# Performance work log

Hardware: AMD Instinct MI355X
Metric: run time of the kernel (lower is better)

Reference implementation:

```python
import jax, jax.numpy as jnp
import numpy as np

N = 50000
E = 800000
EPS = 1e-5


def graph_conv(x, src, dst, ew, W_rel, b_rel, W_root):
    # PyG GraphConv (aggr='add'): lin_rel(sum_j e_ij * x_j) + lin_root(x_i)
    msg = x[src] * ew[:, None]                      # [E, F_in]
    agg = jax.ops.segment_sum(msg, dst, num_segments=N)  # [N, F_in]
    return agg @ W_rel.T + b_rel + x @ W_root.T


def batchnorm_relu(h, gamma, beta):
    mu = jnp.mean(h, axis=0)
    var = jnp.mean(jnp.square(h - mu), axis=0)
    hn = (h - mu) * jax.lax.rsqrt(var + EPS)
    return jax.nn.relu(hn * gamma + beta)


def setup_inputs() -> dict:
    key = jax.random.key(0)
    ks = jax.random.split(key, 16)
    d_in, h, d_out = 128, 256, 64

    def lin(k, fo, fi):
        return jax.random.normal(k, (fo, fi), jnp.float32) * (1.0 / np.sqrt(fi))

    return {
        "x": jax.random.normal(ks[0], (N, d_in), jnp.float32),
        "edge_index": jax.random.randint(ks[1], (2, E), 0, N, jnp.int32),
        "edge_weight": jax.random.uniform(ks[2], (E,), jnp.float32),
        "Wr0": lin(ks[3], h, d_in), "br0": jnp.zeros((h,), jnp.float32), "Wt0": lin(ks[4], h, d_in),
        "g0": jnp.ones((h,), jnp.float32), "be0": jnp.zeros((h,), jnp.float32),
        "Wr1": lin(ks[5], h, h), "br1": jnp.zeros((h,), jnp.float32), "Wt1": lin(ks[6], h, h),
        "g1": jnp.ones((h,), jnp.float32), "be1": jnp.zeros((h,), jnp.float32),
        "Wr2": lin(ks[7], d_out, h), "br2": jnp.zeros((d_out,), jnp.float32), "Wt2": lin(ks[8], d_out, h),
    }


def reference(x, edge_index, edge_weight, Wr0, br0, Wt0, g0, be0,
              Wr1, br1, Wt1, g1, be1, Wr2, br2, Wt2):
    src, dst = edge_index[0], edge_index[1]
    h = graph_conv(x, src, dst, edge_weight, Wr0, br0, Wt0)
    h = batchnorm_relu(h, g0, be0)
    h = graph_conv(h, src, dst, edge_weight, Wr1, br1, Wt1)
    h = batchnorm_relu(h, g1, be1)
    return graph_conv(h, src, dst, edge_weight, Wr2, br2, Wt2)
```

## Files before the change

### kernel.cpp

```cpp
#include <hip/hip_runtime.h>
#include <cstddef>
#include <cstdint>

#define SCAN_B 512

using bf16x8 = __attribute__((ext_vector_type(8))) short;
using f32x4  = __attribute__((ext_vector_type(4))) float;

__device__ __forceinline__ unsigned short f2bf(float f) {
    unsigned int u = __builtin_bit_cast(unsigned int, f);
    return (unsigned short)((u + 0x7FFFu + ((u >> 16) & 1u)) >> 16);
}
__device__ __forceinline__ float bf2f(unsigned short b) {
    unsigned int u = ((unsigned int)b) << 16;
    return __builtin_bit_cast(float, u);
}
__device__ __forceinline__ float i2f(int i) { return __builtin_bit_cast(float, i); }
__device__ __forceinline__ float u2f(unsigned int u) { return __builtin_bit_cast(float, u); }
__device__ __forceinline__ void gload_lds16(const void* g, void* l) {
    __builtin_amdgcn_global_load_lds((const __attribute__((address_space(1))) void*)g,
                                     (__attribute__((address_space(3))) void*)l, 16, 0, 0);
}

__global__ void hist_conv_k(const int* __restrict__ dst, int* __restrict__ counts,
                            int* __restrict__ rank, int E, int histBlocks,
                            const float* __restrict__ x, const float* __restrict__ Wr0,
                            const float* __restrict__ Wt0, const float* __restrict__ Wr1,
                            const float* __restrict__ Wt1, const float* __restrict__ Wr2,
                            const float* __restrict__ Wt2, unsigned short* __restrict__ x_bf,
                            unsigned short* __restrict__ Wr0b, unsigned short* __restrict__ Wt0b,
                            unsigned short* __restrict__ Wr1b, unsigned short* __restrict__ Wt1b,
                            unsigned short* __restrict__ Wr2b, unsigned short* __restrict__ Wt2b,
                            int n4x) {
    if ((int)blockIdx.x < histBlocks) {
        int e = blockIdx.x * 256 + threadIdx.x;
        if (e < E) rank[e] = atomicAdd(&counts[dst[e]], 1);
        return;
    }
    int j = (blockIdx.x - histBlocks) * 256 + threadIdx.x;
    const float* s;
    unsigned short* d;
    if (j < n4x) { s = x; d = x_bf; }
    else {
        j -= n4x;
        if (j < 8192) { s = Wr0; d = Wr0b; }
        else { j -= 8192;
        if (j < 8192) { s = Wt0; d = Wt0b; }
        else { j -= 8192;
        if (j < 16384) { s = Wr1; d = Wr1b; }
        else { j -= 16384;
        if (j < 16384) { s = Wt1; d = Wt1b; }
        else { j -= 16384;
        if (j < 4096) { s = Wr2; d = Wr2b; }
        else { j -= 4096;
        if (j >= 4096) return;
        s = Wt2; d = Wt2b; } } } } }
    }
    float4 v = reinterpret_cast<const float4*>(s)[j];
    ushort4 o;
    o.x = f2bf(v.x); o.y = f2bf(v.y); o.z = f2bf(v.z); o.w = f2bf(v.w);
    reinterpret_cast<ushort4*>(d)[j] = o;
}

__global__ void scan1_k(const int* __restrict__ counts, int* __restrict__ partial,
                        int* __restrict__ blocksum, int Nn) {
    __shared__ int sh[SCAN_B];
    int i = blockIdx.x * SCAN_B + threadIdx.x;
    int v = (i < Nn) ? counts[i] : 0;
    sh[threadIdx.x] = v;
    __syncthreads();
    for (int off = 1; off < SCAN_B; off <<= 1) {
        int t = (threadIdx.x >= (unsigned)off) ? sh[threadIdx.x - off] : 0;
        __syncthreads();
        sh[threadIdx.x] += t;
        __syncthreads();
    }
    if (i < Nn) partial[i] = sh[threadIdx.x];
    if (threadIdx.x == SCAN_B - 1) blocksum[blockIdx.x] = sh[threadIdx.x];
}

__global__ void scan2_k(int* __restrict__ blocksum, int nb) {
    __shared__ int sh[256];
    int v = (threadIdx.x < (unsigned)nb) ? blocksum[threadIdx.x] : 0;
    sh[threadIdx.x] = v;
    __syncthreads();
    for (int off = 1; off < 256; off <<= 1) {
        int t = (threadIdx.x >= (unsigned)off) ? sh[threadIdx.x - off] : 0;
        __syncthreads();
        sh[threadIdx.x] += t;
        __syncthreads();
    }
    if (threadIdx.x < (unsigned)nb) blocksum[threadIdx.x] = sh[threadIdx.x];
}

__global__ void scan3_k(const int* __restrict__ partial, const int* __restrict__ blocksum,
                        int* __restrict__ offsets, int Nn) {
    int i = blockIdx.x * SCAN_B + threadIdx.x;
    if (i >= Nn) return;
    int add = (blockIdx.x > 0) ? blocksum[blockIdx.x - 1] : 0;
    offsets[i + 1] = partial[i] + add;
    if (i == 0) offsets[0] = 0;
}

__global__ void fill2_k(const int* __restrict__ src, const int* __restrict__ dst,
                        const float* __restrict__ ew, const int* __restrict__ offsets,
                        const int* __restrict__ rank, int2* __restrict__ e_sw, int E) {
    int e = blockIdx.x * blockDim.x + threadIdx.x;
    if (e >= E) return;
    int d = dst[e];
    int pos = offsets[d] + rank[e];
    e_sw[pos] = make_int2(src[e], __builtin_bit_cast(int, ew[e]));
}

template<int F>
__global__ void gather_bf_k(const unsigned short* __restrict__ x, const int* __restrict__ offsets,
                            const int2* __restrict__ e_sw, unsigned short* __restrict__ agg, int Nn) {
    int wid = __builtin_amdgcn_readfirstlane((blockIdx.x * blockDim.x + threadIdx.x) >> 6);
    int lane = threadIdx.x & 63;
    if (wid >= Nn) return;
    int p = offsets[wid], end = offsets[wid + 1];
    const char* xb = (const char*)x;
    if constexpr (F == 256) {
        const unsigned loff = lane * 8u;
        float a0 = 0.f, a1 = 0.f, a2 = 0.f, a3 = 0.f;
        for (; p + 8 <= end; p += 8) {
            int2 ee[8];
            #pragma unroll
            for (int i = 0; i < 8; ++i) ee[i] = e_sw[p + i];
            uint2 vv[8];
            #pragma unroll
            for (int i = 0; i < 8; ++i)
                vv[i] = *reinterpret_cast<const uint2*>(xb + ((unsigned)ee[i].x * 512u + loff));
            #pragma unroll
            for (int i = 0; i < 8; ++i) {
                float w = i2f(ee[i].y);
                a0 += w * u2f(vv[i].x << 16); a1 += w * u2f(vv[i].x & 0xFFFF0000u);
                a2 += w * u2f(vv[i].y << 16); a3 += w * u2f(vv[i].y & 0xFFFF0000u);
            }
        }
        for (; p < end; ++p) {
            int2 e0 = e_sw[p];
            uint2 v0 = *reinterpret_cast<const uint2*>(xb + ((unsigned)e0.x * 512u + loff));
            float w = i2f(e0.y);
            a0 += w * u2f(v0.x << 16); a1 += w * u2f(v0.x & 0xFFFF0000u);
            a2 += w * u2f(v0.y << 16); a3 += w * u2f(v0.y & 0xFFFF0000u);
        }
        uint2 o;
        o.x = (unsigned)f2bf(a0) | ((unsigned)f2bf(a1) << 16);
        o.y = (unsigned)f2bf(a2) | ((unsigned)f2bf(a3) << 16);
        *reinterpret_cast<uint2*>(agg + (size_t)wid * 256 + lane * 4) = o;
    } else {
        const unsigned loff = lane * 4u;
        float a0 = 0.f, a1 = 0.f;
        for (; p + 8 <= end; p += 8) {
            int2 ee[8];
            #pragma unroll
            for (int i = 0; i < 8; ++i) ee[i] = e_sw[p + i];
            unsigned vv[8];
            #pragma unroll
            for (int i = 0; i < 8; ++i)
                vv[i] = *reinterpret_cast<const unsigned*>(xb + ((unsigned)ee[i].x * 256u + loff));
            #pragma unroll
            for (int i = 0; i < 8; ++i) {
                float w = i2f(ee[i].y);
                a0 += w * u2f(vv[i] << 16); a1 += w * u2f(vv[i] & 0xFFFF0000u);
            }
        }
        for (; p < end; ++p) {
            int2 e0 = e_sw[p];
            unsigned v0 = *reinterpret_cast<const unsigned*>(xb + ((unsigned)e0.x * 256u + loff));
            float w = i2f(e0.y);
            a0 += w * u2f(v0 << 16); a1 += w * u2f(v0 & 0xFFFF0000u);
        }
        unsigned o = (unsigned)f2bf(a0) | ((unsigned)f2bf(a1) << 16);
        *reinterpret_cast<unsigned*>(agg + (size_t)wid * 128 + lane * 2) = o;
    }
}

__global__ void gather_out_k(const unsigned short* __restrict__ t, const float* __restrict__ root,
                             const int* __restrict__ offsets, const int2* __restrict__ e_sw,
                             float* __restrict__ out, int Nn) {
    int gt = blockIdx.x * blockDim.x + threadIdx.x;
    int node = gt >> 4;
    int li = gt & 15;
    if (node >= Nn) return;
    int p = offsets[node], end = offsets[node + 1];
    const char* tb = (const char*)t;
    const unsigned loff = li * 8u;
    float a0 = 0.f, a1 = 0.f, a2 = 0.f, a3 = 0.f;
    for (; p + 8 <= end; p += 8) {
        int2 ee[8];
        #pragma unroll
        for (int i = 0; i < 8; ++i) ee[i] = e_sw[p + i];
        uint2 vv[8];
        #pragma unroll
        for (int i = 0; i < 8; ++i)
            vv[i] = *reinterpret_cast<const uint2*>(tb + ((unsigned)ee[i].x * 128u + loff));
        #pragma unroll
        for (int i = 0; i < 8; ++i) {
            float w = i2f(ee[i].y);
            a0 += w * u2f(vv[i].x << 16); a1 += w * u2f(vv[i].x & 0xFFFF0000u);
            a2 += w * u2f(vv[i].y << 16); a3 += w * u2f(vv[i].y & 0xFFFF0000u);
        }
    }
    for (; p < end; ++p) {
        int2 e0 = e_sw[p];
        uint2 v0 = *reinterpret_cast<const uint2*>(tb + ((unsigned)e0.x * 128u + loff));
        float w = i2f(e0.y);
        a0 += w * u2f(v0.x << 16); a1 += w * u2f(v0.x & 0xFFFF0000u);
        a2 += w * u2f(v0.y << 16); a3 += w * u2f(v0.y & 0xFFFF0000u);
    }
    float4 r = *reinterpret_cast<const float4*>(root + (size_t)node * 64 + li * 4);
    float4 o = make_float4(r.x + a0, r.y + a1, r.z + a2, r.w + a3);
    *reinterpret_cast<float4*>(out + (size_t)node * 64 + li * 4) = o;
}

template<int K, int O, int BM, int BN, int MODE>
__global__ __launch_bounds__(512, 4) void gemm_mfma_k(
        const unsigned short* __restrict__ A, const unsigned short* __restrict__ Wa,
        const unsigned short* __restrict__ X, const unsigned short* __restrict__ Wb,
        const float* __restrict__ bias, unsigned short* __restrict__ out_bf,
        float* __restrict__ out_f, float* __restrict__ sums, float* __restrict__ sumsq,
        int Nn) {
    constexpr int MI = BM / 32;
    constexpr int OJ = BN / 64;
    constexpr int KSTEPS = K / 64;
    constexpr int NT = (MODE == 0 ? 2 : 1) * KSTEPS;
    constexpr int ACH = BM / 64;
    constexpr int BCH = BN / 64;
    __shared__ unsigned short As[2][BM * 64];
    __shared__ unsigned short Bs[2][BN * 64];
    const int tid = threadIdx.x;
    const int w = tid >> 6, l = tid & 63;
    const int wr = w >> 2, wc = w & 3;
    const int lrow = l & 15, kgrp = l >> 4;
    int bx = blockIdx.x;
    bx = (bx & 7) * (gridDim.x >> 3) + (bx >> 3);
    const int m0 = bx * BM;
    const int n0 = blockIdx.y * BN;

    auto stage = [&](int buf, int t) {
        int ph = t / KSTEPS;
        int k0 = (t % KSTEPS) * 64;
        const unsigned short* Ap = (MODE == 0 && ph) ? X : A;
        const unsigned short* Wp = (MODE == 0 && ph) ? Wb : Wa;
        #pragma unroll
        for (int i = 0; i < ACH; ++i) {
            int c = i * 512 + tid;
            int row = c >> 3, slot = c & 7;
            gload_lds16(Ap + (size_t)(m0 + row) * K + k0 + ((slot ^ (row & 7)) << 3),
                        &As[buf][(i * 512 + w * 64) * 8]);
        }
        #pragma unroll
        for (int i = 0; i < BCH; ++i) {
            int c = i * 512 + tid;
            int row = c >> 3, slot = c & 7;
            gload_lds16(Wp + (size_t)(n0 + row) * K + k0 + ((slot ^ (row & 7)) << 3),
                        &Bs[buf][(i * 512 + w * 64) * 8]);
        }
    };

    f32x4 acc[MI][OJ];
    #pragma unroll
    for (int i = 0; i < MI; ++i)
        #pragma unroll
        for (int j = 0; j < OJ; ++j) {
            f32x4 z = {0.f, 0.f, 0.f, 0.f};
            acc[i][j] = z;
        }

    stage(0, 0);
    __syncthreads();
    #pragma unroll
    for (int t = 0; t < NT; ++t) {
        const int cur = t & 1;
        if (t + 1 < NT) stage(cur ^ 1, t + 1);
        #pragma unroll
        for (int ks = 0; ks < 2; ++ks) {
            bf16x8 a[MI], b[OJ];
            #pragma unroll
            for (int mi = 0; mi < MI; ++mi) {
                int row = wr * 64 + mi * 16 + lrow;
                int slot = (ks * 4 + kgrp) ^ (row & 7);
                a[mi] = *reinterpret_cast<const bf16x8*>(&As[cur][row * 64 + slot * 8]);
            }
            #pragma unroll
            for (int oj = 0; oj < OJ; ++oj) {
                int row = wc * 32 + oj * 16 + lrow;
                int slot = (ks * 4 + kgrp) ^ (row & 7);
                b[oj] = *reinterpret_cast<const bf16x8*>(&Bs[cur][row * 64 + slot * 8]);
            }
            #pragma unroll
            for (int mi = 0; mi < MI; ++mi)
                #pragma unroll
                for (int oj = 0; oj < OJ; ++oj)
                    acc[mi][oj] = __builtin_amdgcn_mfma_f32_16x16x32_bf16(
                        a[mi], b[oj], acc[mi][oj], 0, 0, 0);
        }
        __syncthreads();
    }

    if constexpr (MODE == 0) {
        #pragma unroll
        for (int oj = 0; oj < OJ; ++oj) {
            int col = n0 + wc * 32 + oj * 16 + lrow;
            float bcol = bias[col];
            float s = 0.f, q = 0.f;
            #pragma unroll
            for (int mi = 0; mi < MI; ++mi) {
                #pragma unroll
                for (int r = 0; r < 4; ++r) {
                    int row = m0 + wr * 64 + mi * 16 + kgrp * 4 + r;
                    float v = acc[mi][oj][r] + bcol;
                    if (row < Nn) {
                        out_bf[(size_t)row * O + col] = f2bf(v);
                        s += v; q += v * v;
                    }
                }
            }
            s += __shfl_xor(s, 16, 64); q += __shfl_xor(q, 16, 64);
            s += __shfl_xor(s, 32, 64); q += __shfl_xor(q, 32, 64);
            if (kgrp == 0) {
                atomicAdd(&sums[col], s);
                atomicAdd(&sumsq[col], q);
            }
        }
    } else {
        #pragma unroll
        for (int oj = 0; oj < OJ; ++oj) {
            int col = n0 + wc * 32 + oj * 16 + lrow;
            #pragma unroll
            for (int mi = 0; mi < MI; ++mi) {
                #pragma unroll
                for (int r = 0; r < 4; ++r) {
                    int row = m0 + wr * 64 + mi * 16 + kgrp * 4 + r;
                    if (row < Nn) {
                        if (col < 64)
                            out_bf[(size_t)row * 64 + col] = f2bf(acc[mi][oj][r]);
                        else
                            out_f[(size_t)row * 64 + (col - 64)] = acc[mi][oj][r] + bias[col - 64];
                    }
                }
            }
        }
    }
}

__global__ void bn_relu_bf_k(const unsigned short* __restrict__ h, const float* __restrict__ sums,
                             const float* __restrict__ sumsq, const float* __restrict__ g,
                             const float* __restrict__ be, unsigned short* __restrict__ hb,
                             float invN, int total4) {
    int t = blockIdx.x * blockDim.x + threadIdx.x;
    if (t >= total4) return;
    int f0 = (t & 63) * 4;
    float4 sm = *reinterpret_cast<const float4*>(sums + f0);
    float4 sq = *reinterpret_cast<const float4*>(sumsq + f0);
    float4 gg = *reinterpret_cast<const float4*>(g + f0);
    float4 bb = *reinterpret_cast<const float4*>(be + f0);
    float smv[4] = {sm.x, sm.y, sm.z, sm.w};
    float sqv[4] = {sq.x, sq.y, sq.z, sq.w};
    float ggv[4] = {gg.x, gg.y, gg.z, gg.w};
    float bbv[4] = {bb.x, bb.y, bb.z, bb.w};
    ushort4 v = reinterpret_cast<const ushort4*>(h)[t];
    unsigned short vv[4] = {v.x, v.y, v.z, v.w};
    ushort4 o;
    unsigned short* op = &o.x;
    #pragma unroll
    for (int c = 0; c < 4; ++c) {
        float mu = smv[c] * invN;
        float var = sqv[c] * invN - mu * mu;
        float sc = ggv[c] * rsqrtf(var + 1e-5f);
        float sh = bbv[c] - mu * sc;
        op[c] = f2bf(fmaxf(bf2f(vv[c]) * sc + sh, 0.f));
    }
    reinterpret_cast<ushort4*>(hb)[t] = o;
}

extern "C" void kernel_launch(void* const* d_in, const int* in_sizes, int n_in,
                              void* d_out, int out_size, void* d_ws, size_t ws_size,
                              hipStream_t stream) {
    const float* x   = (const float*)d_in[0];
    const int*   ei  = (const int*)d_in[1];
    const float* ew  = (const float*)d_in[2];
    const float* Wr0 = (const float*)d_in[3];
    const float* br0 = (const float*)d_in[4];
    const float* Wt0 = (const float*)d_in[5];
    const float* g0  = (const float*)d_in[6];
    const float* be0 = (const float*)d_in[7];
    const float* Wr1 = (const float*)d_in[8];
    const float* br1 = (const float*)d_in[9];
    const float* Wt1 = (const float*)d_in[10];
    const float* g1  = (const float*)d_in[11];
    const float* be1 = (const float*)d_in[12];
    const float* Wr2 = (const float*)d_in[13];
    const float* br2 = (const float*)d_in[14];
    const float* Wt2 = (const float*)d_in[15];

    const int E  = in_sizes[2];
    const int Nn = in_sizes[0] / 128;
    const size_t NP = 50176;
    const int* src = ei;
    const int* dst = ei + E;

    unsigned short* x_bf   = (unsigned short*)d_ws;
    unsigned short* agg_bf = x_bf + NP * 128;
    unsigned short* h0N    = agg_bf + NP * 256;
    unsigned short* h1N    = h0N + NP * 256;
    unsigned short* h_bf   = h1N + NP * 256;
    unsigned short* t_bf   = h_bf + NP * 256;
    unsigned short* wbf    = t_bf + NP * 64;
    unsigned short* Wr0b = wbf;
    unsigned short* Wt0b = wbf + 32768;
    unsigned short* Wr1b = wbf + 65536;
    unsigned short* Wt1b = wbf + 131072;
    unsigned short* W2cat = wbf + 196608;
    float* root  = (float*)(wbf + 229376);
    int2*  e_sw  = (int2*)(root + NP * 64);
    float* stats = (float*)(e_sw + E);
    int*   counts  = (int*)(stats + 4096);
    int*   partial = counts + Nn;
    int*   blocksum = partial + Nn;
    int*   rank    = blocksum + 512;
    int*   offsets = rank + E;

    dim3 blk(256);
    const int nbScan = (Nn + SCAN_B - 1) / SCAN_B;
    const float invN = 1.0f / (float)Nn;
    const int n4x = Nn * 32;
    const int histBlocks = (E + 255) / 256;
    const int convBlocks = (n4x + 57344 + 255) / 256;

    hipMemsetAsync(stats, 0, (4096 + (size_t)Nn) * sizeof(float), stream);

    hist_conv_k<<<dim3(histBlocks + convBlocks), blk, 0, stream>>>(
        dst, counts, rank, E, histBlocks,
        x, Wr0, Wt0, Wr1, Wt1, Wr2, Wt2,
        x_bf, Wr0b, Wt0b, Wr1b, Wt1b, W2cat, W2cat + 16384, n4x);
    scan1_k<<<dim3(nbScan), dim3(SCAN_B), 0, stream>>>(counts, partial, blocksum, Nn);
    scan2_k<<<dim3(1), dim3(256), 0, stream>>>(blocksum, nbScan);
    scan3_k<<<dim3(nbScan), dim3(SCAN_B), 0, stream>>>(partial, blocksum, offsets, Nn);
    fill2_k<<<dim3(histBlocks), blk, 0, stream>>>(src, dst, ew, offsets, rank, e_sw, E);

    const int gatherBlocks = (Nn * 64 + 255) / 256;

    gather_bf_k<128><<<dim3(gatherBlocks), blk, 0, stream>>>(x_bf, offsets, e_sw, agg_bf, Nn);
    gemm_mfma_k<128, 256, 128, 128, 0><<<dim3(NP / 128, 2), dim3(512), 0, stream>>>(
        agg_bf, Wr0b, x_bf, Wt0b, br0, h_bf, nullptr, stats + 0, stats + 256, Nn);
    bn_relu_bf_k<<<dim3((Nn * 64 + 255) / 256), blk, 0, stream>>>(
        h_bf, stats + 0, stats + 256, g0, be0, h0N, invN, Nn * 64);

    gather_bf_k<256><<<dim3(gatherBlocks), blk, 0, stream>>>(h0N, offsets, e_sw, agg_bf, Nn);
    gemm_mfma_k<256, 256, 128, 128, 0><<<dim3(NP / 128, 2), dim3(512), 0, stream>>>(
        agg_bf, Wr1b, h0N, Wt1b, br1, h_bf, nullptr, stats + 1024, stats + 1280, Nn);
    bn_relu_bf_k<<<dim3((Nn * 64 + 255) / 256), blk, 0, stream>>>(
        h_bf, stats + 1024, stats + 1280, g1, be1, h1N, invN, Nn * 64);

    gemm_mfma_k<256, 128, 128, 128, 1><<<dim3(NP / 128, 1), dim3(512), 0, stream>>>(
        h1N, W2cat, nullptr, nullptr, br2, t_bf, root, nullptr, nullptr, Nn);
    gather_out_k<<<dim3((Nn * 16 + 255) / 256), blk, 0, stream>>>(
        t_bf, root, offsets, e_sw, (float*)d_out, Nn);
}
```

Before: 304.6 us.

## Fuse BN-ReLU into layer-1 gather, merge scan kernels, shrink GEMM K-tile

The second and third scan kernels become one, with each block summing the preceding block totals itself. The layer-0 BN+ReLU is folded into the layer-1 gather, which normalizes neighbor rows on the fly, while extra blocks in the same launch write the normalized h0N needed by the root GEMM. The GEMM K-step drops from 64 to 32, using half the LDS, one 16-byte load per thread per operand, and a new XOR swizzle. This removes two launches and a dependent read of h0N before the gather, at the cost of recomputing BN per edge element and running more, shorter K iterations with more barriers.

```diff
diff --git a/kernel.cpp b/kernel.cpp
--- a/kernel.cpp
+++ b/kernel.cpp
@@ -79,26 +79,21 @@
     if (threadIdx.x == SCAN_B - 1) blocksum[blockIdx.x] = sh[threadIdx.x];
 }
 
-__global__ void scan2_k(int* __restrict__ blocksum, int nb) {
-    __shared__ int sh[256];
-    int v = (threadIdx.x < (unsigned)nb) ? blocksum[threadIdx.x] : 0;
-    sh[threadIdx.x] = v;
+__global__ void scan3b_k(const int* __restrict__ partial, const int* __restrict__ blocksum,
+                         int* __restrict__ offsets, int Nn) {
+    __shared__ int add_s;
+    int bx = blockIdx.x;
+    if (threadIdx.x < 64) {
+        int s = 0;
+        for (int j = threadIdx.x; j < bx; j += 64) s += blocksum[j];
+        #pragma unroll
+        for (int off = 32; off > 0; off >>= 1) s += __shfl_down(s, off, 64);
+        if (threadIdx.x == 0) add_s = s;
+    }
     __syncthreads();
-    for (int off = 1; off < 256; off <<= 1) {
-        int t = (threadIdx.x >= (unsigned)off) ? sh[threadIdx.x - off] : 0;
-        __syncthreads();
-        sh[threadIdx.x] += t;
-        __syncthreads();
-    }
-    if (threadIdx.x < (unsigned)nb) blocksum[threadIdx.x] = sh[threadIdx.x];
-}
-
-__global__ void scan3_k(const int* __restrict__ partial, const int* __restrict__ blocksum,
-                        int* __restrict__ offsets, int Nn) {
-    int i = blockIdx.x * SCAN_B + threadIdx.x;
+    int i = bx * SCAN_B + threadIdx.x;
     if (i >= Nn) return;
-    int add = (blockIdx.x > 0) ? blocksum[blockIdx.x - 1] : 0;
-    offsets[i + 1] = partial[i] + add;
+    offsets[i + 1] = partial[i] + add_s;
     if (i == 0) offsets[0] = 0;
 }
 
@@ -107,74 +102,128 @@
                         const int* __restrict__ rank, int2* __restrict__ e_sw, int E) {
     int e = blockIdx.x * blockDim.x + threadIdx.x;
     if (e >= E) return;
-    int d = dst[e];
-    int pos = offsets[d] + rank[e];
+    int pos = offsets[dst[e]] + rank[e];
     e_sw[pos] = make_int2(src[e], __builtin_bit_cast(int, ew[e]));
 }
 
-template<int F>
-__global__ void gather_bf_k(const unsigned short* __restrict__ x, const int* __restrict__ offsets,
+__global__ void gather128_k(const unsigned short* __restrict__ x, const int* __restrict__ offsets,
                             const int2* __restrict__ e_sw, unsigned short* __restrict__ agg, int Nn) {
     int wid = __builtin_amdgcn_readfirstlane((blockIdx.x * blockDim.x + threadIdx.x) >> 6);
     int lane = threadIdx.x & 63;
     if (wid >= Nn) return;
     int p = offsets[wid], end = offsets[wid + 1];
     const char* xb = (const char*)x;
-    if constexpr (F == 256) {
-        const unsigned loff = lane * 8u;
-        float a0 = 0.f, a1 = 0.f, a2 = 0.f, a3 = 0.f;
-        for (; p + 8 <= end; p += 8) {
-            int2 ee[8];
+    const unsigned loff = lane * 4u;
+    float a0 = 0.f, a1 = 0.f;
+    for (; p + 8 <= end; p += 8) {
+        int2 ee[8];
+        #pragma unroll
+        for (int i = 0; i < 8; ++i) ee[i] = e_sw[p + i];
+        unsigned vv[8];
+        #pragma unroll
+        for (int i = 0; i < 8; ++i)
+            vv[i] = *reinterpret_cast<const unsigned*>(xb + ((unsigned)ee[i].x * 256u + loff));
+        #pragma unroll
+        for (int i = 0; i < 8; ++i) {
+            float w = i2f(ee[i].y);
+            a0 += w * u2f(vv[i] << 16); a1 += w * u2f(vv[i] & 0xFFFF0000u);
+        }
+    }
+    for (; p < end; ++p) {
+        int2 e0 = e_sw[p];
+        unsigned v0 = *reinterpret_cast<const unsigned*>(xb + ((unsigned)e0.x * 256u + loff));
+        float w = i2f(e0.y);
+        a0 += w * u2f(v0 << 16); a1 += w * u2f(v0 & 0xFFFF0000u);
+    }
+    unsigned o = (unsigned)f2bf(a0) | ((unsigned)f2bf(a1) << 16);
+    *reinterpret_cast<unsigned*>(agg + (size_t)wid * 128 + lane * 2) = o;
+}
+
+__global__ void gather_bn_k(const unsigned short* __restrict__ h_raw,
+                            const float* __restrict__ sums, const float* __restrict__ sumsq,
+                            const float* __restrict__ g, const float* __restrict__ be,
+                            const int* __restrict__ offsets, const int2* __restrict__ e_sw,
+                            unsigned short* __restrict__ agg, unsigned short* __restrict__ hN,
+                            float invN, int Nn, int gBlocks) {
+    const int lane = threadIdx.x & 63;
+    if ((int)blockIdx.x >= gBlocks) {
+        int total4 = Nn * 64;
+        int stride = (gridDim.x - gBlocks) * 256;
+        for (int t = (blockIdx.x - gBlocks) * 256 + threadIdx.x; t < total4; t += stride) {
+            int f0 = (t & 63) * 4;
+            float4 sm = *reinterpret_cast<const float4*>(sums + f0);
+            float4 sq = *reinterpret_cast<const float4*>(sumsq + f0);
+            float4 gg = *reinterpret_cast<const float4*>(g + f0);
+            float4 bb = *reinterpret_cast<const float4*>(be + f0);
+            float smv[4] = {sm.x, sm.y, sm.z, sm.w};
+            float sqv[4] = {sq.x, sq.y, sq.z, sq.w};
+            float ggv[4] = {gg.x, gg.y, gg.z, gg.w};
+            float bbv[4] = {bb.x, bb.y, bb.z, bb.w};
+            ushort4 v = reinterpret_cast<const ushort4*>(h_raw)[t];
+            unsigned short vv[4] = {v.x, v.y, v.z, v.w};
+            ushort4 o;
+            unsigned short* op = &o.x;
             #pragma unroll
-            for (int i = 0; i < 8; ++i) ee[i] = e_sw[p + i];
-            uint2 vv[8];
-            #pragma unroll
-            for (int i = 0; i < 8; ++i)
-                vv[i] = *reinterpret_cast<const uint2*>(xb + ((unsigned)ee[i].x * 512u + loff));
-            #pragma unroll
-            for (int i = 0; i < 8; ++i) {
-                float w = i2f(ee[i].y);
-                a0 += w * u2f(vv[i].x << 16); a1 += w * u2f(vv[i].x & 0xFFFF0000u);
-                a2 += w * u2f(vv[i].y << 16); a3 += w * u2f(vv[i].y & 0xFFFF0000u);
+            for (int c = 0; c < 4; ++c) {
+                float mu = smv[c] * invN;
+                float var = sqv[c] * invN - mu * mu;
+                float sc = ggv[c] * rsqrtf(var + 1e-5f);
+                float sh = bbv[c] - mu * sc;
+                op[c] = f2bf(fmaxf(bf2f(vv[c]) * sc + sh, 0.f));
             }
-        }
-        for (; p < end; ++p) {
-            int2 e0 = e_sw[p];
-            uint2 v0 = *reinterpret_cast<const uint2*>(xb + ((unsigned)e0.x * 512u + loff));
-            float w = i2f(e0.y);
-            a0 += w * u2f(v0.x << 16); a1 += w * u2f(v0.x & 0xFFFF0000u);
-            a2 += w * u2f(v0.y << 16); a3 += w * u2f(v0.y & 0xFFFF0000u);
-        }
-        uint2 o;
-        o.x = (unsigned)f2bf(a0) | ((unsigned)f2bf(a1) << 16);
-        o.y = (unsigned)f2bf(a2) | ((unsigned)f2bf(a3) << 16);
-        *reinterpret_cast<uint2*>(agg + (size_t)wid * 256 + lane * 4) = o;
-    } else {
-        const unsigned loff = lane * 4u;
-        float a0 = 0.f, a1 = 0.f;
-        for (; p + 8 <= end; p += 8) {
-            int2 ee[8];
-            #pragma unroll
-            for (int i = 0; i < 8; ++i) ee[i] = e_sw[p + i];
-            unsigned vv[8];
-            #pragma unroll
-            for (int i = 0; i < 8; ++i)
-                vv[i] = *reinterpret_cast<const unsigned*>(xb + ((unsigned)ee[i].x * 256u + loff));
-            #pragma unroll
-            for (int i = 0; i < 8; ++i) {
-                float w = i2f(ee[i].y);
-                a0 += w * u2f(vv[i] << 16); a1 += w * u2f(vv[i] & 0xFFFF0000u);
-            }
-        }
-        for (; p < end; ++p) {
-            int2 e0 = e_sw[p];
-            unsigned v0 = *reinterpret_cast<const unsigned*>(xb + ((unsigned)e0.x * 256u + loff));
-            float w = i2f(e0.y);
-            a0 += w * u2f(v0 << 16); a1 += w * u2f(v0 & 0xFFFF0000u);
-        }
-        unsigned o = (unsigned)f2bf(a0) | ((unsigned)f2bf(a1) << 16);
-        *reinterpret_cast<unsigned*>(agg + (size_t)wid * 128 + lane * 2) = o;
-    }
+            reinterpret_cast<ushort4*>(hN)[t] = o;
+        }
+        return;
+    }
+    int wid = __builtin_amdgcn_readfirstlane((blockIdx.x * blockDim.x + threadIdx.x) >> 6);
+    if (wid >= Nn) return;
+    int f0 = lane * 4;
+    float4 sm = *reinterpret_cast<const float4*>(sums + f0);
+    float4 sq = *reinterpret_cast<const float4*>(sumsq + f0);
+    float4 gg = *reinterpret_cast<const float4*>(g + f0);
+    float4 bb = *reinterpret_cast<const float4*>(be + f0);
+    float sc0, sc1, sc2, sc3, sh0, sh1, sh2, sh3;
+    {
+        float mu, var;
+        mu = sm.x * invN; var = sq.x * invN - mu * mu; sc0 = gg.x * rsqrtf(var + 1e-5f); sh0 = bb.x - mu * sc0;
+        mu = sm.y * invN; var = sq.y * invN - mu * mu; sc1 = gg.y * rsqrtf(var + 1e-5f); sh1 = bb.y - mu * sc1;
+        mu = sm.z * invN; var = sq.z * invN - mu * mu; sc2 = gg.z * rsqrtf(var + 1e-5f); sh2 = bb.z - mu * sc2;
+        mu = sm.w * invN; var = sq.w * invN - mu * mu; sc3 = gg.w * rsqrtf(var + 1e-5f); sh3 = bb.w - mu * sc3;
+    }
+    int p = offsets[wid], end = offsets[wid + 1];
+    const char* xb = (const char*)h_raw;
+    const unsigned loff = lane * 8u;
+    float a0 = 0.f, a1 = 0.f, a2 = 0.f, a3 = 0.f;
+    for (; p + 8 <= end; p += 8) {
+        int2 ee[8];
+        #pragma unroll
+        for (int i = 0; i < 8; ++i) ee[i] = e_sw[p + i];
+        uint2 vv[8];
+        #pragma unroll
+        for (int i = 0; i < 8; ++i)
+            vv[i] = *reinterpret_cast<const uint2*>(xb + ((unsigned)ee[i].x * 512u + loff));
+        #pragma unroll
+        for (int i = 0; i < 8; ++i) {
+            float w = i2f(ee[i].y);
+            a0 += w * fmaxf(u2f(vv[i].x << 16) * sc0 + sh0, 0.f);
+            a1 += w * fmaxf(u2f(vv[i].x & 0xFFFF0000u) * sc1 + sh1, 0.f);
+            a2 += w * fmaxf(u2f(vv[i].y << 16) * sc2 + sh2, 0.f);
+            a3 += w * fmaxf(u2f(vv[i].y & 0xFFFF0000u) * sc3 + sh3, 0.f);
+        }
+    }
+    for (; p < end; ++p) {
+        int2 e0 = e_sw[p];
+        uint2 v0 = *reinterpret_cast<const uint2*>(xb + ((unsigned)e0.x * 512u + loff));
+        float w = i2f(e0.y);
+        a0 += w * fmaxf(u2f(v0.x << 16) * sc0 + sh0, 0.f);
+        a1 += w * fmaxf(u2f(v0.x & 0xFFFF0000u) * sc1 + sh1, 0.f);
+        a2 += w * fmaxf(u2f(v0.y << 16) * sc2 + sh2, 0.f);
+        a3 += w * fmaxf(u2f(v0.y & 0xFFFF0000u) * sc3 + sh3, 0.f);
+    }
+    uint2 o;
+    o.x = (unsigned)f2bf(a0) | ((unsigned)f2bf(a1) << 16);
+    o.y = (unsigned)f2bf(a2) | ((unsigned)f2bf(a3) << 16);
+    *reinterpret_cast<uint2*>(agg + (size_t)wid * 256 + lane * 4) = o;
 }
 
 __global__ void gather_out_k(const unsigned short* __restrict__ t, const float* __restrict__ root,
@@ -215,21 +264,20 @@
     *reinterpret_cast<float4*>(out + (size_t)node * 64 + li * 4) = o;
 }
 
-template<int K, int O, int BM, int BN, int MODE>
+template<int K, int O, int MODE>
 __global__ __launch_bounds__(512, 4) void gemm_mfma_k(
         const unsigned short* __restrict__ A, const unsigned short* __restrict__ Wa,
         const unsigned short* __restrict__ X, const unsigned short* __restrict__ Wb,
         const float* __restrict__ bias, unsigned short* __restrict__ out_bf,
         float* __restrict__ out_f, float* __restrict__ sums, float* __restrict__ sumsq,
         int Nn) {
-    constexpr int MI = BM / 32;
-    constexpr int OJ = BN / 64;
-    constexpr int KSTEPS = K / 64;
+    constexpr int BM = 128, BN = 128;
+    constexpr int MI = 4;
+    constexpr int OJ = 2;
+    constexpr int KSTEPS = K / 32;
     constexpr int NT = (MODE == 0 ? 2 : 1) * KSTEPS;
-    constexpr int ACH = BM / 64;
-    constexpr int BCH = BN / 64;
-    __shared__ unsigned short As[2][BM * 64];
-    __shared__ unsigned short Bs[2][BN * 64];
+    __shared__ unsigned short As[2][BM * 32];
+    __shared__ unsigned short Bs[2][BN * 32];
     const int tid = threadIdx.x;
     const int w = tid >> 6, l = tid & 63;
     const int wr = w >> 2, wc = w & 3;
@@ -238,26 +286,16 @@
     bx = (bx & 7) * (gridDim.x >> 3) + (bx >> 3);
     const int m0 = bx * BM;
     const int n0 = blockIdx.y * BN;
+    const int srow = tid >> 2, sslot = tid & 3;
+    const int gslot = sslot ^ ((srow >> 1) & 3);
 
     auto stage = [&](int buf, int t) {
         int ph = t / KSTEPS;
-        int k0 = (t % KSTEPS) * 64;
+        int k0 = (t % KSTEPS) * 32;
         const unsigned short* Ap = (MODE == 0 && ph) ? X : A;
         const unsigned short* Wp = (MODE == 0 && ph) ? Wb : Wa;
-        #pragma unroll
-        for (int i = 0; i < ACH; ++i) {
-            int c = i * 512 + tid;
-            int row = c >> 3, slot = c & 7;
-            gload_lds16(Ap + (size_t)(m0 + row) * K + k0 + ((slot ^ (row & 7)) << 3),
-                        &As[buf][(i * 512 + w * 64) * 8]);
-        }
-        #pragma unroll
-        for (int i = 0; i < BCH; ++i) {
-            int c = i * 512 + tid;
-            int row = c >> 3, slot = c & 7;
-            gload_lds16(Wp + (size_t)(n0 + row) * K + k0 + ((slot ^ (row & 7)) << 3),
-                        &Bs[buf][(i * 512 + w * 64) * 8]);
-        }
+        gload_lds16(Ap + (size_t)(m0 + srow) * K + k0 + (gslot << 3), &As[buf][w * 512]);
+        gload_lds16(Wp + (size_t)(n0 + srow) * K + k0 + (gslot << 3), &Bs[buf][w * 512]);
     };
 
     f32x4 acc[MI][OJ];
@@ -275,28 +313,25 @@
     for (int t = 0; t < NT; ++t) {
         const int cur = t & 1;
         if (t + 1 < NT) stage(cur ^ 1, t + 1);
-        #pragma unroll
-        for (int ks = 0; ks < 2; ++ks) {
-            bf16x8 a[MI], b[OJ];
+        bf16x8 a[MI], b[OJ];
+        #pragma unroll
+        for (int mi = 0; mi < MI; ++mi) {
+            int row = wr * 64 + mi * 16 + lrow;
+            int slot = kgrp ^ ((row >> 1) & 3);
+            a[mi] = *reinterpret_cast<const bf16x8*>(&As[cur][row * 32 + slot * 8]);
+        }
+        #pragma unroll
+        for (int oj = 0; oj < OJ; ++oj) {
+            int row = wc * 32 + oj * 16 + lrow;
+            int slot = kgrp ^ ((row >> 1) & 3);
+            b[oj] = *reinterpret_cast<const bf16x8*>(&Bs[cur][row * 32 + slot * 8]);
+        }
+        #pragma unroll
+        for (int mi = 0; mi < MI; ++mi)
             #pragma unroll
-            for (int mi = 0; mi < MI; ++mi) {
-                int row = wr * 64 + mi * 16 + lrow;
-                int slot = (ks * 4 + kgrp) ^ (row & 7);
-                a[mi] = *reinterpret_cast<const bf16x8*>(&As[cur][row * 64 + slot * 8]);
-            }
-            #pragma unroll
-            for (int oj = 0; oj < OJ; ++oj) {
-                int row = wc * 32 + oj * 16 + lrow;
-                int slot = (ks * 4 + kgrp) ^ (row & 7);
-                b[oj] = *reinterpret_cast<const bf16x8*>(&Bs[cur][row * 64 + slot * 8]);
-            }
-            #pragma unroll
-            for (int mi = 0; mi < MI; ++mi)
-                #pragma unroll
-                for (int oj = 0; oj < OJ; ++oj)
-                    acc[mi][oj] = __builtin_amdgcn_mfma_f32_16x16x32_bf16(
-                        a[mi], b[oj], acc[mi][oj], 0, 0, 0);
-        }
+            for (int oj = 0; oj < OJ; ++oj)
+                acc[mi][oj] = __builtin_amdgcn_mfma_f32_16x16x32_bf16(
+                    a[mi], b[oj], acc[mi][oj], 0, 0, 0);
         __syncthreads();
     }
 
@@ -437,25 +472,25 @@
         x, Wr0, Wt0, Wr1, Wt1, Wr2, Wt2,
         x_bf, Wr0b, Wt0b, Wr1b, Wt1b, W2cat, W2cat + 16384, n4x);
     scan1_k<<<dim3(nbScan), dim3(SCAN_B), 0, stream>>>(counts, partial, blocksum, Nn);
-    scan2_k<<<dim3(1), dim3(256), 0, stream>>>(blocksum, nbScan);
-    scan3_k<<<dim3(nbScan), dim3(SCAN_B), 0, stream>>>(partial, blocksum, offsets, Nn);
+    scan3b_k<<<dim3(nbScan), dim3(SCAN_B), 0, stream>>>(partial, blocksum, offsets, Nn);
     fill2_k<<<dim3(histBlocks), blk, 0, stream>>>(src, dst, ew, offsets, rank, e_sw, E);
 
     const int gatherBlocks = (Nn * 64 + 255) / 256;
 
-    gather_bf_k<128><<<dim3(gatherBlocks), blk, 0, stream>>>(x_bf, offsets, e_sw, agg_bf, Nn);
-    gemm_mfma_k<128, 256, 128, 128, 0><<<dim3(NP / 128, 2), dim3(512), 0, stream>>>(
+    gather128_k<<<dim3(gatherBlocks), blk, 0, stream>>>(x_bf, offsets, e_sw, agg_bf, Nn);
+    gemm_mfma_k<128, 256, 0><<<dim3(NP / 128, 2), dim3(512), 0, stream>>>(
         agg_bf, Wr0b, x_bf, Wt0b, br0, h_bf, nullptr, stats + 0, stats + 256, Nn);
-    bn_relu_bf_k<<<dim3((Nn * 64 + 255) / 256), blk, 0, stream>>>(
-        h_bf, stats + 0, stats + 256, g0, be0, h0N, invN, Nn * 64);
-
-    gather_bf_k<256><<<dim3(gatherBlocks), blk, 0, stream>>>(h0N, offsets, e_sw, agg_bf, Nn);
-    gemm_mfma_k<256, 256, 128, 128, 0><<<dim3(NP / 128, 2), dim3(512), 0, stream>>>(
+
+    gather_bn_k<<<dim3(gatherBlocks + 2048), blk, 0, stream>>>(
+        h_bf, stats + 0, stats + 256, g0, be0, offsets, e_sw,
+        agg_bf, h0N, invN, Nn, gatherBlocks);
+
+    gemm_mfma_k<256, 256, 0><<<dim3(NP / 128, 2), dim3(512), 0, stream>>>(
         agg_bf, Wr1b, h0N, Wt1b, br1, h_bf, nullptr, stats + 1024, stats + 1280, Nn);
     bn_relu_bf_k<<<dim3((Nn * 64 + 255) / 256), blk, 0, stream>>>(
         h_bf, stats + 1024, stats + 1280, g1, be1, h1N, invN, Nn * 64);
 
-    gemm_mfma_k<256, 128, 128, 128, 1><<<dim3(NP / 128, 1), dim3(512), 0, stream>>>(
+    gemm_mfma_k<256, 128, 1><<<dim3(NP / 128, 1), dim3(512), 0, stream>>>(
         h1N, W2cat, nullptr, nullptr, br2, t_bf, root, nullptr, nullptr, Nn);
     gather_out_k<<<dim3((Nn * 16 + 255) / 256), blk, 0, stream>>>(
         t_bf, root, offsets, e_sw, (float*)d_out, Nn);
```

Result: faster. 295.9 us (-2.9%).
